# Performance work log

Hardware: AMD Instinct MI355X
Metric: run time of the kernel (lower is better)

The kernel has to match this reference:

```python
import math
import jax, jax.numpy as jnp
import numpy as np

N_FFT = 1024
HOP = 320
WIN = 800
SR = 32000
N_MELS = 128
FMIN = 0.0
FMAX = SR / 2.0
NUM_BINS = N_FFT // 2 + 1  # 513
PREEMPH = 0.97


def _hann_window(n):
    # torch.hann_window(n, periodic=False): 0.5 - 0.5*cos(2*pi*i/(n-1))
    i = np.arange(n, dtype=np.float64)
    return (0.5 - 0.5 * np.cos(2.0 * np.pi * i / (n - 1))).astype(np.float32)


def _fourier_basis():
    offset = (N_FFT - WIN) // 2
    win_full = np.zeros(N_FFT, dtype=np.float64)
    win_full[offset:offset + WIN] = _hann_window(WIN)
    n = np.arange(N_FFT, dtype=np.float64)[None, :]
    k = np.arange(NUM_BINS, dtype=np.float64)[:, None]
    ang = 2.0 * np.pi * k * (n / float(N_FFT))
    cos_k = np.cos(ang) * win_full
    sin_k = -np.sin(ang) * win_full
    return np.concatenate([cos_k, sin_k], axis=0).astype(np.float32)  # [2*513, 1024]


def _kaldi_mel_banks():
    # torchaudio.compliance.kaldi.get_mel_banks with vtln_warp_factor=1.0
    num_fft_bins = N_FFT // 2
    fft_bin_width = SR / float(N_FFT)
    mel = lambda f: 1127.0 * np.log(1.0 + f / 700.0)
    mel_low, mel_high = mel(FMIN), mel(FMAX)
    delta = (mel_high - mel_low) / (N_MELS + 1)
    left = mel_low + np.arange(N_MELS, dtype=np.float64) * delta  # [M]
    right = left + 2.0 * delta
    freqs = fft_bin_width * np.arange(num_fft_bins, dtype=np.float64)
    m = mel(freqs)[None, :]  # [1, 512]
    up = (m - left[:, None]) / delta
    down = (right[:, None] - m) / delta
    bank = np.maximum(0.0, np.minimum(up, down))  # [128, 512]
    bank = np.pad(bank, ((0, 0), (0, 1)))  # pad one zero column -> [128, 513]
    return bank.astype(np.float32)


def setup_inputs() -> dict:
    key = jax.random.key(0)
    x = jax.random.normal(key, (32, 320000), dtype=jnp.float32)
    return {
        "x": x,
        "fourier_basis": jnp.asarray(_fourier_basis()),
        "mel_basis": jnp.asarray(_kaldi_mel_banks()),
    }


def reference(x, fourier_basis, mel_basis):
    # preemphasis: conv1d with kernel [-0.97, 1.0] (cross-correlation)
    y = x[:, 1:] - PREEMPH * x[:, :-1]  # [B, T-1]
    # center pad by n_fft//2
    pad = N_FFT // 2
    y = jnp.pad(y, ((0, 0), (pad, pad)))
    Tp = y.shape[1]
    frames = (Tp - N_FFT) // HOP + 1
    # frame extraction: [B, frames, n_fft]
    idx = jnp.arange(frames)[:, None] * HOP + jnp.arange(N_FFT)[None, :]
    f = y[:, idx]
    # explicit DFT via dense matmul: [B, 2*num_bins, frames]
    spec = jnp.einsum('btn,cn->bct', f, fourier_basis)
    real = spec[:, :NUM_BINS, :]
    imag = spec[:, NUM_BINS:, :]
    power = real * real + imag * imag  # [B, num_bins, frames]
    mel = jnp.einsum('mf,bft->bmt', mel_basis, power)
    log_mel = (jnp.log(mel + 1e-05) + 4.5) / 5.0
    return log_mel
```

## Files before the change

kernel.cpp:

```cpp
#include <hip/hip_runtime.h>
#include <math.h>

typedef _Float16 half8 __attribute__((ext_vector_type(8)));
typedef float f32x4 __attribute__((ext_vector_type(4)));

constexpr int kNFFT    = 1024;
constexpr int kHop     = 320;
constexpr int kMels    = 128;
constexpr int kFrames  = 1000;
constexpr int kBatch   = 32;
constexpr int kXLen    = 320000;
constexpr int kYLen    = kXLen - 1;
constexpr int kYPad    = 328704;
constexpr int kYOff    = 512;
constexpr float kPre   = 0.97f;
constexpr int kPStride = 544;

constexpr size_t kYLvl     = (size_t)kBatch * kYPad;
constexpr size_t kFragLvl  = 64ull * 32 * 64 * 8;
constexpr size_t kFragOff  = 2 * kYLvl;
constexpr size_t kMelFrOff = kFragOff + 2 * kFragLvl;
constexpr size_t kMelFrSz  = 8ull * 17 * 64 * 8;
constexpr size_t kPowOff   = kMelFrOff + kMelFrSz;
constexpr size_t kPowSz    = (size_t)kBatch * 1024 * kPStride;

struct alignas(8) h4 { _Float16 v[4]; };

__global__ void prep_y(const float* __restrict__ x, _Float16* __restrict__ yp) {
    int i = blockIdx.x * 256 + threadIdx.x;
    if (i >= kYPad) return;
    int b = blockIdx.y;
    int yi = i - kYOff;
    float v = 0.0f;
    if (yi >= 0 && yi < kYLen) {
        const float* xb = x + (size_t)b * kXLen;
        v = xb[yi + 1] - kPre * xb[yi];
    }
    _Float16 h = (_Float16)v;
    _Float16 m = (_Float16)(v - (float)h);
    size_t idx = (size_t)b * kYPad + i;
    yp[idx] = h;
    yp[idx + kYLvl] = m;
}

__global__ void prep_frags(const float* __restrict__ basis, _Float16* __restrict__ fr) {
    int id = blockIdx.x * 256 + threadIdx.x;
    int L  = id & 63;
    int ks = (id >> 6) & 31;
    int g  = id >> 11;
    int r  = 16 * g + (L & 15);
    int orig = (r <= 512) ? r : r + 1;
    const float* src = basis + (size_t)orig * kNFFT + 32 * ks + (L >> 4) * 8;
    _Float16* dst = fr + (size_t)id * 8;
    #pragma unroll
    for (int j = 0; j < 8; ++j) {
        float a = src[j];
        _Float16 h = (_Float16)a;
        _Float16 m = (_Float16)(a - (float)h);
        dst[j] = h;
        dst[j + kFragLvl] = m;
    }
}

__global__ void prep_melfr(const float* __restrict__ melb, _Float16* __restrict__ fr) {
    int id = blockIdx.x * 256 + threadIdx.x;
    if (id >= 8 * 17 * 64) return;
    int f = id / 1088;
    int rem = id - f * 1088;
    int ks = rem >> 6;
    int L = rem & 63;
    int m = 16 * f + (L & 15);
    int kb = 32 * ks + (L >> 4) * 8;
    _Float16* dst = fr + (size_t)id * 8;
    #pragma unroll
    for (int j = 0; j < 8; ++j) {
        int k = kb + j;
        dst[j] = (k < 513) ? (_Float16)melb[(size_t)m * 513 + k] : (_Float16)0.0f;
    }
}

__global__ __launch_bounds__(256, 2)
void stft_power(const _Float16* __restrict__ frags,
                const _Float16* __restrict__ ypad,
                _Float16* __restrict__ pw) {
    __shared__ __align__(16) _Float16 ash[16 * 512];
    const int tid  = threadIdx.x;
    const int w    = tid >> 6;
    const int lane = tid & 63;
    const int quad = lane >> 4;
    const int l16  = lane & 15;
    const int nt = blockIdx.x, g = blockIdx.y, b = blockIdx.z;
    const int t0 = nt * 256 + w * 64;

    const _Float16* yb0 = ypad + (size_t)b * kYPad;
    const _Float16* yb1 = yb0 + kYLvl;

    f32x4 acc[8][4] = {};

    for (int ks = 0; ks < 32; ++ks) {
        __syncthreads();
        #pragma unroll
        for (int c = 0; c < 4; ++c) {
            int slot = w + 4 * c;
            int f = slot & 7;
            int lv = slot >> 3;
            int Gf = (f < 4) ? (4 * g + f) : (32 + 4 * g + (f - 4));
            const _Float16* gp = frags + (size_t)lv * kFragLvl
                                 + ((size_t)(Gf * 32 + ks) * 64 + lane) * 8;
            __builtin_amdgcn_global_load_lds(
                (const __attribute__((address_space(1))) void*)gp,
                (__attribute__((address_space(3))) void*)&ash[slot * 512],
                16, 0, 0);
        }
        half8 bh[4], bm[4];
        #pragma unroll
        for (int nf = 0; nf < 4; ++nf) {
            int off = (t0 + nf * 16 + l16) * kHop + ks * 32 + quad * 8;
            bh[nf] = *(const half8*)(yb0 + off);
            bm[nf] = *(const half8*)(yb1 + off);
        }
        __syncthreads();
        #pragma unroll
        for (int f = 0; f < 8; ++f) {
            half8 afh = *(const half8*)&ash[f * 512 + lane * 8];
            half8 afm = *(const half8*)&ash[(8 + f) * 512 + lane * 8];
            #pragma unroll
            for (int nf = 0; nf < 4; ++nf) {
                f32x4 a = acc[f][nf];
                a = __builtin_amdgcn_mfma_f32_16x16x32_f16(afh, bh[nf], a, 0, 0, 0);
                a = __builtin_amdgcn_mfma_f32_16x16x32_f16(afh, bm[nf], a, 0, 0, 0);
                a = __builtin_amdgcn_mfma_f32_16x16x32_f16(afm, bh[nf], a, 0, 0, 0);
                acc[f][nf] = a;
            }
        }
    }

    #pragma unroll
    for (int mf = 0; mf < 4; ++mf) {
        int b0 = 64 * g + 16 * mf + 4 * quad;
        #pragma unroll
        for (int nf = 0; nf < 4; ++nf) {
            int t = t0 + nf * 16 + l16;
            size_t row = ((size_t)((b << 10) + t)) * kPStride;
            h4 pp;
            #pragma unroll
            for (int r = 0; r < 4; ++r) {
                float pA = acc[mf][nf][r];
                float pB = acc[4 + mf][nf][r];
                float p2 = pA * pA + pB * pB;
                if (g == 0 && mf == 0 && quad == 0 && r == 0) {
                    p2 = pA * pA;
                    pw[row + 512] = (_Float16)(pB * pB);
                }
                pp.v[r] = (_Float16)p2;
            }
            *(h4*)&pw[row + b0] = pp;
        }
    }
}

__global__ __launch_bounds__(256)
void mel_mfma(const _Float16* __restrict__ melfr, const _Float16* __restrict__ pw,
              float* __restrict__ out) {
    const int tid  = threadIdx.x;
    const int w    = tid >> 6;
    const int lane = tid & 63;
    const int quad = lane >> 4;
    const int l16  = lane & 15;
    const int nt = blockIdx.x, b = blockIdx.y;
    const int t0 = nt * 128 + w * 32;

    f32x4 acc[8][2] = {};
    for (int ks = 0; ks < 17; ++ks) {
        half8 bp[2];
        #pragma unroll
        for (int nf = 0; nf < 2; ++nf) {
            int t = t0 + nf * 16 + l16;
            bp[nf] = *(const half8*)(pw + ((size_t)((b << 10) + t)) * kPStride
                                     + 32 * ks + quad * 8);
        }
        #pragma unroll
        for (int f = 0; f < 8; ++f) {
            half8 af = *(const half8*)(melfr + ((size_t)(f * 17 + ks) * 64 + lane) * 8);
            #pragma unroll
            for (int nf = 0; nf < 2; ++nf)
                acc[f][nf] = __builtin_amdgcn_mfma_f32_16x16x32_f16(af, bp[nf], acc[f][nf], 0, 0, 0);
        }
    }
    #pragma unroll
    for (int f = 0; f < 8; ++f) {
        #pragma unroll
        for (int nf = 0; nf < 2; ++nf) {
            int t = t0 + nf * 16 + l16;
            if (t < kFrames) {
                #pragma unroll
                for (int r = 0; r < 4; ++r) {
                    int m = 16 * f + 4 * quad + r;
                    out[((size_t)(b * kMels + m)) * kFrames + t] =
                        (__logf(acc[f][nf][r] + 1e-5f) + 4.5f) * 0.2f;
                }
            }
        }
    }
}

extern "C" void kernel_launch(void* const* d_in, const int* in_sizes, int n_in,
                              void* d_out, int out_size, void* d_ws, size_t ws_size,
                              hipStream_t stream) {
    const float* x     = (const float*)d_in[0];
    const float* basis = (const float*)d_in[1];
    const float* melb  = (const float*)d_in[2];
    float* out = (float*)d_out;

    _Float16* ws    = (_Float16*)d_ws;
    _Float16* ypad  = ws;
    _Float16* frags = ws + kFragOff;
    _Float16* melfr = ws + kMelFrOff;
    _Float16* pw    = ws + kPowOff;

    prep_y<<<dim3((kYPad + 255) / 256, kBatch), 256, 0, stream>>>(x, ypad);
    prep_frags<<<dim3(131072 / 256), 256, 0, stream>>>(basis, frags);
    prep_melfr<<<dim3((8 * 17 * 64 + 255) / 256), 256, 0, stream>>>(melb, melfr);
    stft_power<<<dim3(4, 8, kBatch), 256, 0, stream>>>(frags, ypad, pw);
    mel_mfma<<<dim3(8, kBatch), 256, 0, stream>>>(melfr, pw, out);
}
```

Before: 276.4 us.

## Double-buffer STFT tiles, widen blocks, vectorize preemphasis, shrink mel tiles

The STFT kernel now runs 512-thread blocks where each wave handles 32 frames instead of 64. The basis fragments in LDS and the frame registers are double-buffered, so the next k-step's global loads overlap the MFMA work on the current step. The preemphasis prep kernel now processes 8 samples per thread using float4 loads and half8 stores, replacing scalar accesses. The mel kernel uses one 16-frame tile per wave over twice as many blocks to raise parallelism, at the cost of reloading the mel fragments more often.

```diff
diff --git a/kernel.cpp b/kernel.cpp
--- a/kernel.cpp
+++ b/kernel.cpp
@@ -22,25 +22,40 @@
 constexpr size_t kMelFrOff = kFragOff + 2 * kFragLvl;
 constexpr size_t kMelFrSz  = 8ull * 17 * 64 * 8;
 constexpr size_t kPowOff   = kMelFrOff + kMelFrSz;
-constexpr size_t kPowSz    = (size_t)kBatch * 1024 * kPStride;
-
-struct alignas(8) h4 { _Float16 v[4]; };
 
 __global__ void prep_y(const float* __restrict__ x, _Float16* __restrict__ yp) {
     int i = blockIdx.x * 256 + threadIdx.x;
-    if (i >= kYPad) return;
+    int e0 = i * 8;
+    if (e0 >= kYPad) return;
     int b = blockIdx.y;
-    int yi = i - kYOff;
-    float v = 0.0f;
-    if (yi >= 0 && yi < kYLen) {
-        const float* xb = x + (size_t)b * kXLen;
-        v = xb[yi + 1] - kPre * xb[yi];
-    }
-    _Float16 h = (_Float16)v;
-    _Float16 m = (_Float16)(v - (float)h);
-    size_t idx = (size_t)b * kYPad + i;
-    yp[idx] = h;
-    yp[idx + kYLvl] = m;
+    const float* xb = x + (size_t)b * kXLen;
+    int yi = e0 - kYOff;
+    float v[8];
+    if (yi >= 0 && yi <= kXLen - 9) {
+        float4 A = *(const float4*)(xb + yi);
+        float4 B = *(const float4*)(xb + yi + 4);
+        float C = xb[yi + 8];
+        v[0] = A.y - kPre * A.x;  v[1] = A.z - kPre * A.y;
+        v[2] = A.w - kPre * A.z;  v[3] = B.x - kPre * A.w;
+        v[4] = B.y - kPre * B.x;  v[5] = B.z - kPre * B.y;
+        v[6] = B.w - kPre * B.z;  v[7] = C   - kPre * B.w;
+    } else {
+        #pragma unroll
+        for (int j = 0; j < 8; ++j) {
+            int g = yi + j;
+            v[j] = (g >= 0 && g < kYLen) ? xb[g + 1] - kPre * xb[g] : 0.0f;
+        }
+    }
+    half8 hv, mv;
+    #pragma unroll
+    for (int j = 0; j < 8; ++j) {
+        _Float16 h = (_Float16)v[j];
+        hv[j] = h;
+        mv[j] = (_Float16)(v[j] - (float)h);
+    }
+    size_t idx = (size_t)b * kYPad + e0;
+    *(half8*)(yp + idx) = hv;
+    *(half8*)(yp + idx + kYLvl) = mv;
 }
 
 __global__ void prep_frags(const float* __restrict__ basis, _Float16* __restrict__ fr) {
@@ -79,70 +94,86 @@
     }
 }
 
-__global__ __launch_bounds__(256, 2)
+__global__ __launch_bounds__(512, 4)
 void stft_power(const _Float16* __restrict__ frags,
                 const _Float16* __restrict__ ypad,
                 _Float16* __restrict__ pw) {
-    __shared__ __align__(16) _Float16 ash[16 * 512];
+    __shared__ __align__(16) _Float16 ash[2][16 * 512];
     const int tid  = threadIdx.x;
     const int w    = tid >> 6;
     const int lane = tid & 63;
     const int quad = lane >> 4;
     const int l16  = lane & 15;
     const int nt = blockIdx.x, g = blockIdx.y, b = blockIdx.z;
-    const int t0 = nt * 256 + w * 64;
-
+    const int t0 = nt * 256 + w * 32;
     const _Float16* yb0 = ypad + (size_t)b * kYPad;
     const _Float16* yb1 = yb0 + kYLvl;
 
-    f32x4 acc[8][4] = {};
-
-    for (int ks = 0; ks < 32; ++ks) {
-        __syncthreads();
-        #pragma unroll
-        for (int c = 0; c < 4; ++c) {
-            int slot = w + 4 * c;
-            int f = slot & 7;
-            int lv = slot >> 3;
+    f32x4 acc[8][2] = {};
+
+    auto stageA = [&](int ks, int pbuf) {
+        #pragma unroll
+        for (int c = 0; c < 2; ++c) {
+            int slot = w + 8 * c;
+            int f = slot & 7, lv = slot >> 3;
             int Gf = (f < 4) ? (4 * g + f) : (32 + 4 * g + (f - 4));
             const _Float16* gp = frags + (size_t)lv * kFragLvl
-                                 + ((size_t)(Gf * 32 + ks) * 64 + lane) * 8;
+                               + ((size_t)(Gf * 32 + ks) * 64 + lane) * 8;
             __builtin_amdgcn_global_load_lds(
                 (const __attribute__((address_space(1))) void*)gp,
-                (__attribute__((address_space(3))) void*)&ash[slot * 512],
+                (__attribute__((address_space(3))) void*)&ash[pbuf][slot * 512],
                 16, 0, 0);
         }
-        half8 bh[4], bm[4];
-        #pragma unroll
-        for (int nf = 0; nf < 4; ++nf) {
+    };
+    auto loadB = [&](int ks, half8* bh, half8* bm) {
+        #pragma unroll
+        for (int nf = 0; nf < 2; ++nf) {
             int off = (t0 + nf * 16 + l16) * kHop + ks * 32 + quad * 8;
             bh[nf] = *(const half8*)(yb0 + off);
             bm[nf] = *(const half8*)(yb1 + off);
         }
-        __syncthreads();
+    };
+    auto compute = [&](int pbuf, half8* bh, half8* bm) {
         #pragma unroll
         for (int f = 0; f < 8; ++f) {
-            half8 afh = *(const half8*)&ash[f * 512 + lane * 8];
-            half8 afm = *(const half8*)&ash[(8 + f) * 512 + lane * 8];
+            half8 afh = *(const half8*)&ash[pbuf][f * 512 + lane * 8];
+            half8 afm = *(const half8*)&ash[pbuf][(8 + f) * 512 + lane * 8];
             #pragma unroll
-            for (int nf = 0; nf < 4; ++nf) {
+            for (int nf = 0; nf < 2; ++nf) {
                 f32x4 a = acc[f][nf];
                 a = __builtin_amdgcn_mfma_f32_16x16x32_f16(afh, bh[nf], a, 0, 0, 0);
+                a = __builtin_amdgcn_mfma_f32_16x16x32_f16(afm, bh[nf], a, 0, 0, 0);
                 a = __builtin_amdgcn_mfma_f32_16x16x32_f16(afh, bm[nf], a, 0, 0, 0);
-                a = __builtin_amdgcn_mfma_f32_16x16x32_f16(afm, bh[nf], a, 0, 0, 0);
                 acc[f][nf] = a;
             }
         }
+    };
+
+    half8 bhA[2], bmA[2], bhB[2], bmB[2];
+    stageA(0, 0);
+    loadB(0, bhA, bmA);
+    for (int kss = 0; kss < 16; ++kss) {
+        int ks = 2 * kss;
+        __syncthreads();
+        stageA(ks + 1, 1);
+        loadB(ks + 1, bhB, bmB);
+        compute(0, bhA, bmA);
+        __syncthreads();
+        if (ks + 2 < 32) {
+            stageA(ks + 2, 0);
+            loadB(ks + 2, bhA, bmA);
+        }
+        compute(1, bhB, bmB);
     }
 
     #pragma unroll
     for (int mf = 0; mf < 4; ++mf) {
         int b0 = 64 * g + 16 * mf + 4 * quad;
         #pragma unroll
-        for (int nf = 0; nf < 4; ++nf) {
+        for (int nf = 0; nf < 2; ++nf) {
             int t = t0 + nf * 16 + l16;
             size_t row = ((size_t)((b << 10) + t)) * kPStride;
-            h4 pp;
+            struct alignas(8) h4 { _Float16 v[4]; } pp;
             #pragma unroll
             for (int r = 0; r < 4; ++r) {
                 float pA = acc[mf][nf][r];
@@ -154,7 +185,7 @@
                 }
                 pp.v[r] = (_Float16)p2;
             }
-            *(h4*)&pw[row + b0] = pp;
+            *(decltype(pp)*)&pw[row + b0] = pp;
         }
     }
 }
@@ -168,37 +199,26 @@
     const int quad = lane >> 4;
     const int l16  = lane & 15;
     const int nt = blockIdx.x, b = blockIdx.y;
-    const int t0 = nt * 128 + w * 32;
-
-    f32x4 acc[8][2] = {};
+    const int t = nt * 64 + w * 16 + l16;
+
+    f32x4 acc[8] = {};
+    const _Float16* prow = pw + ((size_t)((b << 10) + t)) * kPStride;
     for (int ks = 0; ks < 17; ++ks) {
-        half8 bp[2];
-        #pragma unroll
-        for (int nf = 0; nf < 2; ++nf) {
-            int t = t0 + nf * 16 + l16;
-            bp[nf] = *(const half8*)(pw + ((size_t)((b << 10) + t)) * kPStride
-                                     + 32 * ks + quad * 8);
-        }
+        half8 bp = *(const half8*)(prow + 32 * ks + quad * 8);
         #pragma unroll
         for (int f = 0; f < 8; ++f) {
             half8 af = *(const half8*)(melfr + ((size_t)(f * 17 + ks) * 64 + lane) * 8);
+            acc[f] = __builtin_amdgcn_mfma_f32_16x16x32_f16(af, bp, acc[f], 0, 0, 0);
+        }
+    }
+    if (t < kFrames) {
+        #pragma unroll
+        for (int f = 0; f < 8; ++f) {
             #pragma unroll
-            for (int nf = 0; nf < 2; ++nf)
-                acc[f][nf] = __builtin_amdgcn_mfma_f32_16x16x32_f16(af, bp[nf], acc[f][nf], 0, 0, 0);
-        }
-    }
-    #pragma unroll
-    for (int f = 0; f < 8; ++f) {
-        #pragma unroll
-        for (int nf = 0; nf < 2; ++nf) {
-            int t = t0 + nf * 16 + l16;
-            if (t < kFrames) {
-                #pragma unroll
-                for (int r = 0; r < 4; ++r) {
-                    int m = 16 * f + 4 * quad + r;
-                    out[((size_t)(b * kMels + m)) * kFrames + t] =
-                        (__logf(acc[f][nf][r] + 1e-5f) + 4.5f) * 0.2f;
-                }
+            for (int r = 0; r < 4; ++r) {
+                int m = 16 * f + 4 * quad + r;
+                out[((size_t)(b * kMels + m)) * kFrames + t] =
+                    (__logf(acc[f][r] + 1e-5f) + 4.5f) * 0.2f;
             }
         }
     }
@@ -218,9 +238,9 @@
     _Float16* melfr = ws + kMelFrOff;
     _Float16* pw    = ws + kPowOff;
 
-    prep_y<<<dim3((kYPad + 255) / 256, kBatch), 256, 0, stream>>>(x, ypad);
+    prep_y<<<dim3(kYPad / 8 / 256 + 1, kBatch), 256, 0, stream>>>(x, ypad);
     prep_frags<<<dim3(131072 / 256), 256, 0, stream>>>(basis, frags);
     prep_melfr<<<dim3((8 * 17 * 64 + 255) / 256), 256, 0, stream>>>(melb, melfr);
-    stft_power<<<dim3(4, 8, kBatch), 256, 0, stream>>>(frags, ypad, pw);
-    mel_mfma<<<dim3(8, kBatch), 256, 0, stream>>>(melfr, pw, out);
-}
+    stft_power<<<dim3(4, 8, kBatch), 512, 0, stream>>>(frags, ypad, pw);
+    mel_mfma<<<dim3(16, kBatch), 256, 0, stream>>>(melfr, pw, out);
+}
```

New measurement: 296.5 us. +7.3%, slower.
